# Kernel optimization log

Measured on AMD Instinct MI355X. Metric: run time of the kernel, lower is better.

## Reference

```python
import jax, jax.numpy as jnp
import numpy as np

FEAT = 256
HID = 256
HEADS = 4
DH = HID // HEADS
SCALE = DH ** (-0.5)


def _linear(x, W, b):
    # torch nn.Linear convention: W is [out, in]
    return jnp.einsum('...i,oi->...o', x, W) + b


def _layernorm(x, gamma, beta, eps=1e-5):
    mu = jnp.mean(x, axis=-1, keepdims=True)
    var = jnp.mean(jnp.square(x - mu), axis=-1, keepdims=True)
    return (x - mu) * jax.lax.rsqrt(var + eps) * gamma + beta


def setup_inputs() -> dict:
    key = jax.random.key(0)
    ks = jax.random.split(key, 16)
    B, N = 4, 2048
    def w(k, shape, fan_in):
        return jax.random.uniform(k, shape, jnp.float32, -1.0, 1.0) / np.sqrt(fan_in)
    return {
        'x0': jax.random.normal(ks[0], (B, N, FEAT), jnp.float32),
        'x1': jax.random.normal(ks[1], (B, N, FEAT), jnp.float32),
        'Wqk': w(ks[2], (HID, FEAT), FEAT), 'bqk': w(ks[3], (HID,), FEAT),
        'Wv': w(ks[4], (HID, FEAT), FEAT), 'bv': w(ks[5], (HID,), FEAT),
        'Wp': w(ks[6], (HID, HID), HID), 'bp': w(ks[7], (HID,), HID),
        'W1': w(ks[8], (FEAT * 2, FEAT + HID), FEAT + HID), 'b1': w(ks[9], (FEAT * 2,), FEAT + HID),
        'gamma': jnp.ones((FEAT * 2,), jnp.float32), 'beta': jnp.zeros((FEAT * 2,), jnp.float32),
        'W2': w(ks[10], (FEAT, FEAT * 2), FEAT * 2), 'b2': w(ks[11], (FEAT,), FEAT * 2),
    }


def _forward(x0, x1, Wqk, bqk, Wv, bv, Wp, bp, W1, b1, gamma, beta, W2, b2):
    B, N0, _ = x0.shape
    N1 = x1.shape[1]

    def heads(t):  # [B, N, HID] -> [B, H, N, DH]
        return t.reshape(t.shape[0], t.shape[1], HEADS, DH).transpose(0, 2, 1, 3)

    qk0 = heads(_linear(x0, Wqk, bqk)) * (SCALE ** 0.5)
    qk1 = heads(_linear(x1, Wqk, bqk)) * (SCALE ** 0.5)
    v0 = heads(_linear(x0, Wv, bv))
    v1 = heads(_linear(x1, Wv, bv))

    sim = jnp.einsum('bhid,bhjd->bhij', qk0, qk1)  # [B,H,N0,N1]
    attn01 = jax.nn.softmax(sim, axis=-1)                      # rows over N1
    attn10 = jax.nn.softmax(sim.transpose(0, 1, 3, 2), axis=-1)  # [B,H,N1,N0], rows over N0

    m0 = jnp.einsum('bhij,bhjd->bhid', attn01, v1)  # [B,H,N0,DH]
    m1 = jnp.einsum('bhij,bhjd->bhid', attn10, v0)  # [B,H,N1,DH]

    def merge(t):  # [B,H,N,DH] -> [B,N,HID]
        return t.transpose(0, 2, 1, 3).reshape(t.shape[0], t.shape[2], HID)

    m0 = _linear(merge(m0), Wp, bp)
    m1 = _linear(merge(m1), Wp, bp)

    def mlp(x, m):
        h = _linear(jnp.concatenate([x, m], axis=-1), W1, b1)
        h = jax.nn.gelu(_layernorm(h, gamma, beta), approximate=False)
        return x + _linear(h, W2, b2)

    return mlp(x0, m0), mlp(x1, m1)


def reference(x0, x1, Wqk, bqk, Wv, bv, Wp, bp, W1, b1, gamma, beta, W2, b2):
    return _forward(x0, x1, Wqk, bqk, Wv, bv, Wp, bp, W1, b1, gamma, beta, W2, b2)
```

## Files before the change

kernel.cpp:

```cpp
#include <hip/hip_runtime.h>
#include <hip/hip_bf16.h>
#include <math.h>

typedef __hip_bfloat16 hbf;
typedef __attribute__((ext_vector_type(8))) short short8;
typedef __attribute__((ext_vector_type(4))) short short4v;
typedef __attribute__((ext_vector_type(4))) float f32x4;

#define ROWS 8192
#define SQSL 0.4246609001440095f
#define COFF 24.0f

__device__ __forceinline__ short f2b(float f) {
    union { hbf h; short s; } u; u.h = __float2bfloat16(f); return u.s;
}
__device__ __forceinline__ float b2f(short s) {
    union { unsigned u; float f; } x;
    x.u = ((unsigned)(unsigned short)s) << 16; return x.f;
}

__global__ __launch_bounds__(256)
void prep(const float* __restrict__ Wqk, const float* __restrict__ Wv,
          const float* __restrict__ Wp, const float* __restrict__ W1,
          const float* __restrict__ W2,
          const float* __restrict__ bp, const float* __restrict__ b1,
          short* __restrict__ wq, short* __restrict__ wv,
          short* __restrict__ w1c, short* __restrict__ w2,
          float* __restrict__ bc)
{
    const int bid = blockIdx.x, tid = threadIdx.x;
    if (bid < 512) {
        const float* src; short* dst; int base; float sc = 1.f;
        if (bid < 64)       { src = Wqk; dst = wq; base = bid;       sc = SQSL; }
        else if (bid < 128) { src = Wv;  dst = wv; base = bid - 64; }
        else if (bid < 384) {
            int i = (bid - 128) * 256 + tid;
            int n = i >> 7, c = (i & 127) * 4;
            if (c < 256) {
                float4 f = ((const float4*)W1)[i];
                short4v s;
                s[0] = f2b(f.x); s[1] = f2b(f.y); s[2] = f2b(f.z); s[3] = f2b(f.w);
                *(short4v*)(w1c + (size_t)n * 512 + c) = s;
            }
            return;
        }
        else                { src = W2;  dst = w2; base = bid - 384; }
        int i = base * 256 + tid;
        float4 f = ((const float4*)src)[i];
        short4v s;
        s[0] = f2b(f.x * sc); s[1] = f2b(f.y * sc);
        s[2] = f2b(f.z * sc); s[3] = f2b(f.w * sc);
        *(short4v*)(dst + (size_t)i * 4) = s;
    } else if (bid < 1024) {
        int n = bid - 512;
        const float* wrow = W1 + (size_t)n * 512 + 256;
        float acc = 0.f;
        for (int k = 0; k < 256; ++k)
            acc += wrow[k] * Wp[(size_t)k * 256 + tid];
        w1c[(size_t)n * 512 + 256 + tid] = f2b(acc);
    } else {
        int n = (bid - 1024) * 256 + tid;
        const float* wrow = W1 + (size_t)n * 512 + 256;
        float acc = b1[n];
        for (int k = 0; k < 256; ++k) acc += wrow[k] * bp[k];
        bc[n] = acc;
    }
}

__global__ __launch_bounds__(256)
void gemm_qkv(const float* __restrict__ x0, const float* __restrict__ x1,
              const short* __restrict__ Wa, const short* __restrict__ Wb,
              const float* __restrict__ bias0, const float* __restrict__ bias1,
              short* __restrict__ qkb, short* __restrict__ vtb)
{
    const int fid  = blockIdx.x + (blockIdx.y << 2);
    const int col0 = (fid >> 8) * 128;
    const int row0 = (fid & 255) * 64;
    const int tid = threadIdx.x;
    const int lane = tid & 63, wave = tid >> 6;
    const int ln = lane & 15, quad = lane >> 4;
    const int wm = wave & 1, wn = wave >> 1;

    __shared__ short smem[64 * 72 + 128 * 72];
    short* As = smem;
    short* Bs = smem + 64 * 72;
    short* Vt = smem;

    const int ar = tid >> 2, ac = tid & 3;

    f32x4 acc[2][4];
    #pragma unroll
    for (int i = 0; i < 2; ++i)
        #pragma unroll
        for (int j = 0; j < 4; ++j) acc[i][j] = {0.f, 0.f, 0.f, 0.f};

    const short* wbase = (col0 < 256) ? Wa + (size_t)col0 * 256
                                      : Wb + (size_t)(col0 - 256) * 256;
    const float* xrow = (row0 + ar < ROWS)
        ? x0 + (size_t)(row0 + ar) * 256
        : x1 + (size_t)(row0 + ar - ROWS) * 256;

    float4 aF[4];
    short8 bR[4];
    #pragma unroll
    for (int i = 0; i < 4; ++i) aF[i] = ((const float4*)(xrow + ac * 16))[i];
    bR[0] = *(const short8*)(wbase + (size_t)ar * 256 + ac * 16);
    bR[1] = *(const short8*)(wbase + (size_t)ar * 256 + ac * 16 + 8);
    bR[2] = *(const short8*)(wbase + (size_t)(ar + 64) * 256 + ac * 16);
    bR[3] = *(const short8*)(wbase + (size_t)(ar + 64) * 256 + ac * 16 + 8);

    for (int k0 = 0; k0 < 256; k0 += 64) {
        {
            short8 s0, s1;
            s0[0] = f2b(aF[0].x); s0[1] = f2b(aF[0].y); s0[2] = f2b(aF[0].z); s0[3] = f2b(aF[0].w);
            s0[4] = f2b(aF[1].x); s0[5] = f2b(aF[1].y); s0[6] = f2b(aF[1].z); s0[7] = f2b(aF[1].w);
            s1[0] = f2b(aF[2].x); s1[1] = f2b(aF[2].y); s1[2] = f2b(aF[2].z); s1[3] = f2b(aF[2].w);
            s1[4] = f2b(aF[3].x); s1[5] = f2b(aF[3].y); s1[6] = f2b(aF[3].z); s1[7] = f2b(aF[3].w);
            *(short8*)&As[ar * 72 + ac * 16]     = s0;
            *(short8*)&As[ar * 72 + ac * 16 + 8] = s1;
        }
        *(short8*)&Bs[ar * 72 + ac * 16]            = bR[0];
        *(short8*)&Bs[ar * 72 + ac * 16 + 8]        = bR[1];
        *(short8*)&Bs[(ar + 64) * 72 + ac * 16]     = bR[2];
        *(short8*)&Bs[(ar + 64) * 72 + ac * 16 + 8] = bR[3];
        __syncthreads();

        if (k0 + 64 < 256) {
            const int kk = k0 + 64 + ac * 16;
            #pragma unroll
            for (int i = 0; i < 4; ++i) aF[i] = ((const float4*)(xrow + kk))[i];
            bR[0] = *(const short8*)(wbase + (size_t)ar * 256 + kk);
            bR[1] = *(const short8*)(wbase + (size_t)ar * 256 + kk + 8);
            bR[2] = *(const short8*)(wbase + (size_t)(ar + 64) * 256 + kk);
            bR[3] = *(const short8*)(wbase + (size_t)(ar + 64) * 256 + kk + 8);
        }

        short8 a[2][2], b[4][2];
        #pragma unroll
        for (int mi = 0; mi < 2; ++mi)
            #pragma unroll
            for (int ks = 0; ks < 2; ++ks)
                a[mi][ks] = *(const short8*)&As[(wm * 32 + mi * 16 + ln) * 72 + ks * 32 + quad * 8];
        #pragma unroll
        for (int nj = 0; nj < 4; ++nj)
            #pragma unroll
            for (int ks = 0; ks < 2; ++ks)
                b[nj][ks] = *(const short8*)&Bs[(wn * 64 + nj * 16 + ln) * 72 + ks * 32 + quad * 8];
        #pragma unroll
        for (int mi = 0; mi < 2; ++mi)
            #pragma unroll
            for (int nj = 0; nj < 4; ++nj) {
                acc[mi][nj] = __builtin_amdgcn_mfma_f32_16x16x32_bf16(
                                  b[nj][0], a[mi][0], acc[mi][nj], 0, 0, 0);
                acc[mi][nj] = __builtin_amdgcn_mfma_f32_16x16x32_bf16(
                                  b[nj][1], a[mi][1], acc[mi][nj], 0, 0, 0);
            }
        __syncthreads();
    }

    if (col0 < 256) {
        #pragma unroll
        for (int nj = 0; nj < 4; ++nj) {
            const int wcol = col0 + wn * 64 + nj * 16 + quad * 4;
            float4 bb = *(const float4*)(bias0 + wcol);
            #pragma unroll
            for (int mi = 0; mi < 2; ++mi) {
                const int tok = row0 + wm * 32 + mi * 16 + ln;
                f32x4 v = acc[mi][nj];
                short4v o;
                o[0] = f2b(fmaf(bb.x, SQSL, v[0]));
                o[1] = f2b(fmaf(bb.y, SQSL, v[1]));
                o[2] = f2b(fmaf(bb.z, SQSL, v[2]));
                o[3] = f2b(fmaf(bb.w, SQSL, v[3]));
                *(short4v*)(qkb + (size_t)tok * 256 + wcol) = o;
            }
        }
    } else {
        #pragma unroll
        for (int nj = 0; nj < 4; ++nj) {
            const int wrel = wn * 64 + nj * 16 + quad * 4;
            float4 bb = *(const float4*)(bias1 + (col0 - 256) + wrel);
            #pragma unroll
            for (int mi = 0; mi < 2; ++mi) {
                const int tl = wm * 32 + mi * 16 + ln;
                f32x4 v = acc[mi][nj];
                Vt[(wrel + 0) * 72 + tl] = f2b(v[0] + bb.x);
                Vt[(wrel + 1) * 72 + tl] = f2b(v[1] + bb.y);
                Vt[(wrel + 2) * 72 + tl] = f2b(v[2] + bb.z);
                Vt[(wrel + 3) * 72 + tl] = f2b(v[3] + bb.w);
            }
        }
        __syncthreads();
        {
            const int g4 = (row0 >> 11) * 4, tc0 = row0 & 2047;
            const int r = tid >> 1, hf = tid & 1;
            const int vcol = (col0 - 256) + r;
            const int hh = vcol >> 6, d = vcol & 63;
            short* dst = vtb + (size_t)((g4 + hh) * 64 + d) * 2048 + tc0 + hf * 32;
            #pragma unroll
            for (int cc = 0; cc < 4; ++cc)
                *(short8*)(dst + cc * 8) = *(const short8*)&Vt[r * 72 + hf * 32 + cc * 8];
        }
    }
}

__global__ __launch_bounds__(128, 2)
void attn8(const short* __restrict__ qkb, const short* __restrict__ vtbuf,
           short* __restrict__ pO0, short* __restrict__ pO1,
           float* __restrict__ l0, float* __restrict__ l1)
{
    const int nfl = blockIdx.x + (blockIdx.y << 4) + (blockIdx.z << 8);
    const int qt  = nfl >> 6;
    const int gg  = nfl & 63;
    const int b    = (gg >> 2) & 3, h = gg & 3;
    const int dir  = gg >> 5;
    const int half = (gg >> 4) & 1;
    const int tid = threadIdx.x;
    const int lane = tid & 63, wave = tid >> 6;
    const int ln   = lane & 15, quad = lane >> 4;

    const int qbase = dir * ROWS + b * 2048;
    const int kbase = (1 - dir) * ROWS + b * 2048;
    const int vg    = ((1 - dir) * 4 + b) * 4 + h;
    const int jlo   = half * 1024, jhi = jlo + 1024;

    short* __restrict__ pO = half ? pO1 : pO0;
    float* __restrict__ lb = half ? l1  : l0;

    __shared__ short QP[128 * 72];
    __shared__ short KS[64 * 72];
    __shared__ short VT[64 * 72];

    const int c = tid & 7, r0 = tid >> 3;
    #pragma unroll
    for (int g = 0; g < 8; ++g) {
        int r = r0 + g * 16;
        *(short8*)&QP[r * 72 + c * 8] =
            *(const short8*)(qkb + (size_t)(qbase + qt * 128 + r) * 256 + h * 64 + c * 8);
    }
    #pragma unroll
    for (int g = 0; g < 4; ++g) {
        int r = r0 + g * 16;
        *(short8*)&KS[r * 72 + c * 8] =
            *(const short8*)(qkb + (size_t)(kbase + jlo + r) * 256 + h * 64 + c * 8);
        *(short8*)&VT[r * 72 + c * 8] =
            *(const short8*)(vtbuf + (size_t)(vg * 64 + r) * 2048 + jlo + c * 8);
    }
    __syncthreads();

    short8 qf[4][2];
    #pragma unroll
    for (int mi = 0; mi < 4; ++mi)
        #pragma unroll
        for (int ks = 0; ks < 2; ++ks)
            qf[mi][ks] = *(const short8*)&QP[(wave * 64 + mi * 16 + ln) * 72
                                             + ks * 32 + quad * 8];

    f32x4 Ot[4][4];
    #pragma unroll
    for (int mi = 0; mi < 4; ++mi)
        #pragma unroll
        for (int dt = 0; dt < 4; ++dt) Ot[mi][dt] = {0.f, 0.f, 0.f, 0.f};
    float lrun[4] = {0.f, 0.f, 0.f, 0.f};

    for (int j0 = jlo; j0 < jhi; j0 += 64) {
        short8 kreg[4], vreg[4];
        const bool more = (j0 + 64) < jhi;
        if (more) {
            #pragma unroll
            for (int g = 0; g < 4; ++g) {
                int r = r0 + g * 16;
                kreg[g] = *(const short8*)(qkb + (size_t)(kbase + j0 + 64 + r) * 256
                                           + h * 64 + c * 8);
                vreg[g] = *(const short8*)(vtbuf + (size_t)(vg * 64 + r) * 2048
                                           + j0 + 64 + c * 8);
            }
        }

        f32x4 St[4][4];
        __builtin_amdgcn_s_setprio(1);
        #pragma unroll
        for (int t = 0; t < 4; ++t) {
            short8 k0 = *(const short8*)&KS[(t * 16 + ln) * 72 + quad * 8];
            short8 k1 = *(const short8*)&KS[(t * 16 + ln) * 72 + 32 + quad * 8];
            #pragma unroll
            for (int mi = 0; mi < 4; ++mi) {
                f32x4 z = {0.f, 0.f, 0.f, 0.f};
                z = __builtin_amdgcn_mfma_f32_16x16x32_bf16(k0, qf[mi][0], z, 0, 0, 0);
                St[mi][t] = __builtin_amdgcn_mfma_f32_16x16x32_bf16(k1, qf[mi][1], z, 0, 0, 0);
            }
        }
        __builtin_amdgcn_s_setprio(0);

        float ss[4] = {0.f, 0.f, 0.f, 0.f};
        #pragma unroll
        for (int mi = 0; mi < 4; ++mi)
            #pragma unroll
            for (int t = 0; t < 4; ++t) {
                float p0 = __builtin_amdgcn_exp2f(St[mi][t][0] - COFF);
                float p1 = __builtin_amdgcn_exp2f(St[mi][t][1] - COFF);
                float p2 = __builtin_amdgcn_exp2f(St[mi][t][2] - COFF);
                float p3 = __builtin_amdgcn_exp2f(St[mi][t][3] - COFF);
                ss[mi] += (p0 + p1) + (p2 + p3);
                unsigned d0 = (__float_as_uint(p0) >> 16) |
                              (__float_as_uint(p1) & 0xffff0000u);
                unsigned d1 = (__float_as_uint(p2) >> 16) |
                              (__float_as_uint(p3) & 0xffff0000u);
                *(int2*)&QP[(wave * 64 + mi * 16 + ln) * 72 + t * 16 + quad * 4] =
                    make_int2((int)d0, (int)d1);
            }
        #pragma unroll
        for (int mi = 0; mi < 4; ++mi) {
            float t = ss[mi];
            t += __shfl_xor(t, 16);
            t += __shfl_xor(t, 32);
            lrun[mi] += t;
        }

        short8 pa[4][2];
        #pragma unroll
        for (int mi = 0; mi < 4; ++mi)
            #pragma unroll
            for (int ks = 0; ks < 2; ++ks)
                pa[mi][ks] = *(const short8*)&QP[(wave * 64 + mi * 16 + ln) * 72
                                                 + ks * 32 + quad * 8];
        __builtin_amdgcn_s_setprio(1);
        #pragma unroll
        for (int dt = 0; dt < 4; ++dt) {
            short8 v0 = *(const short8*)&VT[(dt * 16 + ln) * 72 + quad * 8];
            short8 v1 = *(const short8*)&VT[(dt * 16 + ln) * 72 + 32 + quad * 8];
            #pragma unroll
            for (int mi = 0; mi < 4; ++mi) {
                Ot[mi][dt] = __builtin_amdgcn_mfma_f32_16x16x32_bf16(
                                 v0, pa[mi][0], Ot[mi][dt], 0, 0, 0);
                Ot[mi][dt] = __builtin_amdgcn_mfma_f32_16x16x32_bf16(
                                 v1, pa[mi][1], Ot[mi][dt], 0, 0, 0);
            }
        }
        __builtin_amdgcn_s_setprio(0);
        __syncthreads();

        if (more) {
            #pragma unroll
            for (int g = 0; g < 4; ++g) {
                int r = r0 + g * 16;
                *(short8*)&KS[r * 72 + c * 8] = kreg[g];
                *(short8*)&VT[r * 72 + c * 8] = vreg[g];
            }
        }
        __syncthreads();
    }

    #pragma unroll
    for (int mi = 0; mi < 4; ++mi) {
        int tok = qbase + qt * 128 + wave * 64 + mi * 16 + ln;
        if (quad == 0) lb[tok] = lrun[mi];
        #pragma unroll
        for (int dt = 0; dt < 4; ++dt) {
            short4v o;
            #pragma unroll
            for (int r = 0; r < 4; ++r) o[r] = f2b(Ot[mi][dt][r]);
            *(short4v*)(pO + (size_t)tok * 256 + h * 64 + dt * 16 + quad * 4) = o;
        }
    }
}

__global__ __launch_bounds__(256)
void mlp_fused(const float* __restrict__ x0, const float* __restrict__ x1,
               const short* __restrict__ pO0, const short* __restrict__ pO1,
               const float* __restrict__ l0, const float* __restrict__ l1,
               const short* __restrict__ w1c, const short* __restrict__ w2,
               const float* __restrict__ bc, const float* __restrict__ gamma,
               const float* __restrict__ beta, const float* __restrict__ b2,
               float* __restrict__ out)
{
    const int tok0 = blockIdx.x * 32;
    const int tid = threadIdx.x;
    const int lane = tid & 63, wave = tid >> 6;
    const int ln = lane & 15, quad = lane >> 4;

    __shared__ short H [32 * 520];
    __shared__ short Bs[256 * 72];
    __shared__ float stats[4][2][32];

    const int br = tid >> 2, bq = tid & 3;
    short8 bp[8];
    auto loadB = [&](const short* W, int rw, int k0) {
        const short* src = W + (size_t)(rw + br) * 512 + k0 + bq * 16;
        #pragma unroll
        for (int q = 0; q < 4; ++q) {
            bp[2 * q]     = *(const short8*)(src + (size_t)q * 64 * 512);
            bp[2 * q + 1] = *(const short8*)(src + (size_t)q * 64 * 512 + 8);
        }
    };
    loadB(w1c, 0, 0);

    {
        const int arow = tid >> 3, ac = tid & 7;
        const int tok = tok0 + arow;
        if (ac < 4) {
            const float* xr = (tok < ROWS ? x0 + (size_t)tok * 256
                                          : x1 + (size_t)(tok - ROWS) * 256) + ac * 64;
            #pragma unroll
            for (int cc = 0; cc < 8; ++cc) {
                float4 f0 = ((const float4*)(xr + cc * 8))[0];
                float4 f1 = ((const float4*)(xr + cc * 8))[1];
                short8 s;
                s[0] = f2b(f0.x); s[1] = f2b(f0.y); s[2] = f2b(f0.z); s[3] = f2b(f0.w);
                s[4] = f2b(f1.x); s[5] = f2b(f1.y); s[6] = f2b(f1.z); s[7] = f2b(f1.w);
                *(short8*)&H[arow * 520 + ac * 64 + cc * 8] = s;
            }
        } else {
            const int vc = (ac - 4) * 64;
            const float inv = __builtin_amdgcn_rcpf(l0[tok] + l1[tok]);
            #pragma unroll
            for (int cc = 0; cc < 8; ++cc) {
                short8 a = *(const short8*)(pO0 + (size_t)tok * 256 + vc + cc * 8);
                short8 b = *(const short8*)(pO1 + (size_t)tok * 256 + vc + cc * 8);
                short8 s;
                #pragma unroll
                for (int j = 0; j < 8; ++j)
                    s[j] = f2b((b2f(a[j]) + b2f(b[j])) * inv);
                *(short8*)&H[arow * 520 + 256 + vc + cc * 8] = s;
            }
        }
    }

    f32x4 acc[2][8];
    #pragma unroll
    for (int i = 0; i < 2; ++i)
        #pragma unroll
        for (int j = 0; j < 8; ++j) acc[i][j] = {0.f, 0.f, 0.f, 0.f};

    __syncthreads();

    for (int k2 = 0; k2 < 8; ++k2) {
        const int k0 = k2 * 64;
        short8 a0[2], a1[2];
        #pragma unroll
        for (int ks = 0; ks < 2; ++ks) {
            a0[ks] = *(const short8*)&H[ln * 520 + k0 + ks * 32 + quad * 8];
            a1[ks] = *(const short8*)&H[(16 + ln) * 520 + k0 + ks * 32 + quad * 8];
        }
        #pragma unroll
        for (int p = 0; p < 2; ++p) {
            #pragma unroll
            for (int q = 0; q < 4; ++q) {
                *(short8*)&Bs[(br + q * 64) * 72 + bq * 16]     = bp[2 * q];
                *(short8*)&Bs[(br + q * 64) * 72 + bq * 16 + 8] = bp[2 * q + 1];
            }
            __syncthreads();
            if (p == 0)          loadB(w1c, 256, k0);
            else if (k2 < 7)     loadB(w1c, 0, k0 + 64);
            #pragma unroll
            for (int nj = 0; nj < 4; ++nj) {
                #pragma unroll
                for (int ks = 0; ks < 2; ++ks) {
                    short8 bf = *(const short8*)&Bs[(wave * 64 + nj * 16 + ln) * 72
                                                    + ks * 32 + quad * 8];
                    acc[0][p * 4 + nj] = __builtin_amdgcn_mfma_f32_16x16x32_bf16(
                                             bf, a0[ks], acc[0][p * 4 + nj], 0, 0, 0);
                    acc[1][p * 4 + nj] = __builtin_amdgcn_mfma_f32_16x16x32_bf16(
                                             bf, a1[ks], acc[1][p * 4 + nj], 0, 0, 0);
                }
            }
            __syncthreads();
        }
    }

    loadB(w2, 0, 0);

    #pragma unroll
    for (int p = 0; p < 2; ++p)
        #pragma unroll
        for (int nj = 0; nj < 4; ++nj) {
            int hcol = p * 256 + wave * 64 + nj * 16 + quad * 4;
            float4 bb = *(const float4*)(bc + hcol);
            acc[0][p * 4 + nj][0] += bb.x; acc[1][p * 4 + nj][0] += bb.x;
            acc[0][p * 4 + nj][1] += bb.y; acc[1][p * 4 + nj][1] += bb.y;
            acc[0][p * 4 + nj][2] += bb.z; acc[1][p * 4 + nj][2] += bb.z;
            acc[0][p * 4 + nj][3] += bb.w; acc[1][p * 4 + nj][3] += bb.w;
        }

    #pragma unroll
    for (int mi = 0; mi < 2; ++mi) {
        float s1 = 0.f, s2 = 0.f;
        #pragma unroll
        for (int j = 0; j < 8; ++j)
            #pragma unroll
            for (int r = 0; r < 4; ++r) {
                float v = acc[mi][j][r];
                s1 += v; s2 += v * v;
            }
        s1 += __shfl_xor(s1, 16); s2 += __shfl_xor(s2, 16);
        s1 += __shfl_xor(s1, 32); s2 += __shfl_xor(s2, 32);
        if (quad == 0) {
            stats[wave][0][mi * 16 + ln] = s1;
            stats[wave][1][mi * 16 + ln] = s2;
        }
    }
    __syncthreads();

    float mean[2], rstd[2];
    #pragma unroll
    for (int mi = 0; mi < 2; ++mi) {
        int t = mi * 16 + ln;
        float s1 = stats[0][0][t] + stats[1][0][t] + stats[2][0][t] + stats[3][0][t];
        float s2 = stats[0][1][t] + stats[1][1][t] + stats[2][1][t] + stats[3][1][t];
        mean[mi] = s1 * (1.f / 512.f);
        float var = s2 * (1.f / 512.f) - mean[mi] * mean[mi];
        rstd[mi] = rsqrtf(var + 1e-5f);
    }

    #pragma unroll
    for (int p = 0; p < 2; ++p)
        #pragma unroll
        for (int nj = 0; nj < 4; ++nj) {
            int hcol = p * 256 + wave * 64 + nj * 16 + quad * 4;
            float4 gm = *(const float4*)(gamma + hcol);
            float4 bt = *(const float4*)(beta + hcol);
            #pragma unroll
            for (int mi = 0; mi < 2; ++mi) {
                short4v o;
                #pragma unroll
                for (int r = 0; r < 4; ++r) {
                    float g = (r == 0) ? gm.x : (r == 1) ? gm.y : (r == 2) ? gm.z : gm.w;
                    float bta = (r == 0) ? bt.x : (r == 1) ? bt.y : (r == 2) ? bt.z : bt.w;
                    float y = (acc[mi][p * 4 + nj][r] - mean[mi]) * rstd[mi] * g + bta;
                    float u = y * fmaf(y * y, 0.0356774081f, 0.7978845608f);
                    float e = __builtin_amdgcn_exp2f(u * -2.8853900818f);
                    o[r] = f2b(y * __builtin_amdgcn_rcpf(1.f + e));
                }
                *(short4v*)&H[(mi * 16 + ln) * 520 + hcol] = o;
            }
        }

    f32x4 acc2[2][4];
    #pragma unroll
    for (int i = 0; i < 2; ++i)
        #pragma unroll
        for (int j = 0; j < 4; ++j) acc2[i][j] = {0.f, 0.f, 0.f, 0.f};

    for (int s = 0; s < 8; ++s) {
        const int k0 = s * 64;
        #pragma unroll
        for (int q = 0; q < 4; ++q) {
            *(short8*)&Bs[(br + q * 64) * 72 + bq * 16]     = bp[2 * q];
            *(short8*)&Bs[(br + q * 64) * 72 + bq * 16 + 8] = bp[2 * q + 1];
        }
        __syncthreads();
        if (s < 7) loadB(w2, 0, k0 + 64);
        short8 h0[2], h1[2];
        #pragma unroll
        for (int ks = 0; ks < 2; ++ks) {
            h0[ks] = *(const short8*)&H[ln * 520 + k0 + ks * 32 + quad * 8];
            h1[ks] = *(const short8*)&H[(16 + ln) * 520 + k0 + ks * 32 + quad * 8];
        }
        #pragma unroll
        for (int nj = 0; nj < 4; ++nj) {
            #pragma unroll
            for (int ks = 0; ks < 2; ++ks) {
                short8 wf = *(const short8*)&Bs[(wave * 64 + nj * 16 + ln) * 72
                                                + ks * 32 + quad * 8];
                acc2[0][nj] = __builtin_amdgcn_mfma_f32_16x16x32_bf16(
                                  wf, h0[ks], acc2[0][nj], 0, 0, 0);
                acc2[1][nj] = __builtin_amdgcn_mfma_f32_16x16x32_bf16(
                                  wf, h1[ks], acc2[1][nj], 0, 0, 0);
            }
        }
        __syncthreads();
    }

    #pragma unroll
    for (int nj = 0; nj < 4; ++nj) {
        int ocol = wave * 64 + nj * 16 + quad * 4;
        float4 bb = *(const float4*)(b2 + ocol);
        #pragma unroll
        for (int mi = 0; mi < 2; ++mi) {
            int tok = tok0 + mi * 16 + ln;
            const float* xr = (tok < ROWS ? x0 + (size_t)tok * 256
                                          : x1 + (size_t)(tok - ROWS) * 256);
            float4 rv = *(const float4*)(xr + ocol);
            float4 o;
            o.x = acc2[mi][nj][0] + bb.x + rv.x;
            o.y = acc2[mi][nj][1] + bb.y + rv.y;
            o.z = acc2[mi][nj][2] + bb.z + rv.z;
            o.w = acc2[mi][nj][3] + bb.w + rv.w;
            *(float4*)(out + (size_t)tok * 256 + ocol) = o;
        }
    }
}

extern "C" void kernel_launch(void* const* d_in, const int* in_sizes, int n_in,
                              void* d_out, int out_size, void* d_ws, size_t ws_size,
                              hipStream_t stream)
{
    const float* x0    = (const float*)d_in[0];
    const float* x1    = (const float*)d_in[1];
    const float* Wqk   = (const float*)d_in[2];
    const float* bqk   = (const float*)d_in[3];
    const float* Wv    = (const float*)d_in[4];
    const float* bv    = (const float*)d_in[5];
    const float* Wp    = (const float*)d_in[6];
    const float* bp    = (const float*)d_in[7];
    const float* W1    = (const float*)d_in[8];
    const float* b1    = (const float*)d_in[9];
    const float* gamma = (const float*)d_in[10];
    const float* beta  = (const float*)d_in[11];
    const float* W2    = (const float*)d_in[12];
    const float* b2    = (const float*)d_in[13];
    float* out = (float*)d_out;

    char* ws = (char*)d_ws;
    const size_t MB = 1024 * 1024;
    short* qkb  = (short*)ws;
    short* vtb  = (short*)(ws + 8  * MB);
    short* pO0  = (short*)(ws + 16 * MB);
    short* pO1  = (short*)(ws + 24 * MB);
    float* l0   = (float*)(ws + 32 * MB);
    float* l1   = l0 + 16384;
    float* bc   = l1 + 16384;
    short* wq   = (short*)(bc + 512);
    short* wv   = wq + 65536;
    short* w1c  = wv + 65536;
    short* w2   = w1c + 262144;

    prep<<<1026, 256, 0, stream>>>(Wqk, Wv, Wp, W1, W2, bp, b1,
                                   wq, wv, w1c, w2, bc);
    gemm_qkv<<<dim3(4, 256), 256, 0, stream>>>(x0, x1, wq, wv, bqk, bv, qkb, vtb);
    attn8<<<dim3(16, 16, 4), 128, 0, stream>>>(qkb, vtb, pO0, pO1, l0, l1);
    mlp_fused<<<512, 256, 0, stream>>>(x0, x1, pO0, pO1, l0, l1, w1c, w2, bc,
                                       gamma, beta, b2, out);
}
```

Baseline: 202.2 us.

## Load GEMM operands directly into registers and compute softmax row sums with MFMA

The QKV projection and both MLP GEMMs stop staging weights and activations through shared memory. Each wave now loads its MFMA fragments straight from global memory into double-buffered registers, which removes most __syncthreads barriers and LDS traffic. The attention kernel drops the constant exp offset and the setprio hints, computes row sums by an MFMA against a ones vector instead of shuffle reductions, and packs bf16 pairs with a perm instruction. QKV blocks are remapped for locality and launch_bounds now request two blocks per CU. The trade-offs are more redundant global loads, higher register pressure, and a possible exp overflow risk now that the offset is gone.

```diff
diff --git a/kernel.cpp b/kernel.cpp
--- a/kernel.cpp
+++ b/kernel.cpp
@@ -9,7 +9,6 @@
 
 #define ROWS 8192
 #define SQSL 0.4246609001440095f
-#define COFF 24.0f
 
 __device__ __forceinline__ short f2b(float f) {
     union { hbf h; short s; } u; u.h = __float2bfloat16(f); return u.s;
@@ -67,95 +66,98 @@
     }
 }
 
-__global__ __launch_bounds__(256)
+__global__ __launch_bounds__(256, 2)
 void gemm_qkv(const float* __restrict__ x0, const float* __restrict__ x1,
               const short* __restrict__ Wa, const short* __restrict__ Wb,
               const float* __restrict__ bias0, const float* __restrict__ bias1,
               short* __restrict__ qkb, short* __restrict__ vtb)
 {
     const int fid  = blockIdx.x + (blockIdx.y << 2);
-    const int col0 = (fid >> 8) * 128;
-    const int row0 = (fid & 255) * 64;
+    const int col0 = ((fid >> 3) & 3) * 128;
+    const int row0 = ((fid & 7) + (fid >> 5) * 8) * 64;
     const int tid = threadIdx.x;
     const int lane = tid & 63, wave = tid >> 6;
     const int ln = lane & 15, quad = lane >> 4;
     const int wm = wave & 1, wn = wave >> 1;
 
-    __shared__ short smem[64 * 72 + 128 * 72];
-    short* As = smem;
-    short* Bs = smem + 64 * 72;
-    short* Vt = smem;
-
-    const int ar = tid >> 2, ac = tid & 3;
-
-    f32x4 acc[2][4];
-    #pragma unroll
-    for (int i = 0; i < 2; ++i)
-        #pragma unroll
-        for (int j = 0; j < 4; ++j) acc[i][j] = {0.f, 0.f, 0.f, 0.f};
-
+    __shared__ short Vt[128 * 72];
+
+    const float* xr[2];
+    #pragma unroll
+    for (int mi = 0; mi < 2; ++mi) {
+        int r = row0 + wm * 32 + mi * 16 + ln;
+        xr[mi] = ((r < ROWS) ? x0 + (size_t)r * 256
+                             : x1 + (size_t)(r - ROWS) * 256) + quad * 8;
+    }
     const short* wbase = (col0 < 256) ? Wa + (size_t)col0 * 256
                                       : Wb + (size_t)(col0 - 256) * 256;
-    const float* xrow = (row0 + ar < ROWS)
-        ? x0 + (size_t)(row0 + ar) * 256
-        : x1 + (size_t)(row0 + ar - ROWS) * 256;
-
-    float4 aF[4];
-    short8 bR[4];
-    #pragma unroll
-    for (int i = 0; i < 4; ++i) aF[i] = ((const float4*)(xrow + ac * 16))[i];
-    bR[0] = *(const short8*)(wbase + (size_t)ar * 256 + ac * 16);
-    bR[1] = *(const short8*)(wbase + (size_t)ar * 256 + ac * 16 + 8);
-    bR[2] = *(const short8*)(wbase + (size_t)(ar + 64) * 256 + ac * 16);
-    bR[3] = *(const short8*)(wbase + (size_t)(ar + 64) * 256 + ac * 16 + 8);
-
-    for (int k0 = 0; k0 < 256; k0 += 64) {
-        {
-            short8 s0, s1;
-            s0[0] = f2b(aF[0].x); s0[1] = f2b(aF[0].y); s0[2] = f2b(aF[0].z); s0[3] = f2b(aF[0].w);
-            s0[4] = f2b(aF[1].x); s0[5] = f2b(aF[1].y); s0[6] = f2b(aF[1].z); s0[7] = f2b(aF[1].w);
-            s1[0] = f2b(aF[2].x); s1[1] = f2b(aF[2].y); s1[2] = f2b(aF[2].z); s1[3] = f2b(aF[2].w);
-            s1[4] = f2b(aF[3].x); s1[5] = f2b(aF[3].y); s1[6] = f2b(aF[3].z); s1[7] = f2b(aF[3].w);
-            *(short8*)&As[ar * 72 + ac * 16]     = s0;
-            *(short8*)&As[ar * 72 + ac * 16 + 8] = s1;
-        }
-        *(short8*)&Bs[ar * 72 + ac * 16]            = bR[0];
-        *(short8*)&Bs[ar * 72 + ac * 16 + 8]        = bR[1];
-        *(short8*)&Bs[(ar + 64) * 72 + ac * 16]     = bR[2];
-        *(short8*)&Bs[(ar + 64) * 72 + ac * 16 + 8] = bR[3];
-        __syncthreads();
-
-        if (k0 + 64 < 256) {
-            const int kk = k0 + 64 + ac * 16;
-            #pragma unroll
-            for (int i = 0; i < 4; ++i) aF[i] = ((const float4*)(xrow + kk))[i];
-            bR[0] = *(const short8*)(wbase + (size_t)ar * 256 + kk);
-            bR[1] = *(const short8*)(wbase + (size_t)ar * 256 + kk + 8);
-            bR[2] = *(const short8*)(wbase + (size_t)(ar + 64) * 256 + kk);
-            bR[3] = *(const short8*)(wbase + (size_t)(ar + 64) * 256 + kk + 8);
-        }
-
-        short8 a[2][2], b[4][2];
+    const short* wr[4];
+    #pragma unroll
+    for (int nj = 0; nj < 4; ++nj)
+        wr[nj] = wbase + (size_t)(wn * 64 + nj * 16 + ln) * 256 + quad * 8;
+
+    f32x4 acc[2][4];
+    #pragma unroll
+    for (int i = 0; i < 2; ++i)
+        #pragma unroll
+        for (int j = 0; j < 4; ++j) acc[i][j] = {0.f, 0.f, 0.f, 0.f};
+
+    float4 aB[2][2][2][2];
+    short8 bB[2][4][2];
+
+    #pragma unroll
+    for (int mi = 0; mi < 2; ++mi)
+        #pragma unroll
+        for (int ks = 0; ks < 2; ++ks) {
+            const float* p = xr[mi] + ks * 32;
+            aB[0][mi][ks][0] = ((const float4*)p)[0];
+            aB[0][mi][ks][1] = ((const float4*)p)[1];
+        }
+    #pragma unroll
+    for (int nj = 0; nj < 4; ++nj)
+        #pragma unroll
+        for (int ks = 0; ks < 2; ++ks)
+            bB[0][nj][ks] = *(const short8*)(wr[nj] + ks * 32);
+
+    #pragma unroll
+    for (int kk = 0; kk < 4; ++kk) {
+        const int cur = kk & 1, nxt = cur ^ 1;
+        if (kk < 3) {
+            const int k0 = (kk + 1) * 64;
+            #pragma unroll
+            for (int mi = 0; mi < 2; ++mi)
+                #pragma unroll
+                for (int ks = 0; ks < 2; ++ks) {
+                    const float* p = xr[mi] + k0 + ks * 32;
+                    aB[nxt][mi][ks][0] = ((const float4*)p)[0];
+                    aB[nxt][mi][ks][1] = ((const float4*)p)[1];
+                }
+            #pragma unroll
+            for (int nj = 0; nj < 4; ++nj)
+                #pragma unroll
+                for (int ks = 0; ks < 2; ++ks)
+                    bB[nxt][nj][ks] = *(const short8*)(wr[nj] + k0 + ks * 32);
+        }
+        short8 a[2][2];
         #pragma unroll
         for (int mi = 0; mi < 2; ++mi)
             #pragma unroll
-            for (int ks = 0; ks < 2; ++ks)
-                a[mi][ks] = *(const short8*)&As[(wm * 32 + mi * 16 + ln) * 72 + ks * 32 + quad * 8];
-        #pragma unroll
-        for (int nj = 0; nj < 4; ++nj)
-            #pragma unroll
-            for (int ks = 0; ks < 2; ++ks)
-                b[nj][ks] = *(const short8*)&Bs[(wn * 64 + nj * 16 + ln) * 72 + ks * 32 + quad * 8];
+            for (int ks = 0; ks < 2; ++ks) {
+                float4 f0 = aB[cur][mi][ks][0], f1 = aB[cur][mi][ks][1];
+                short8 s;
+                s[0] = f2b(f0.x); s[1] = f2b(f0.y); s[2] = f2b(f0.z); s[3] = f2b(f0.w);
+                s[4] = f2b(f1.x); s[5] = f2b(f1.y); s[6] = f2b(f1.z); s[7] = f2b(f1.w);
+                a[mi][ks] = s;
+            }
         #pragma unroll
         for (int mi = 0; mi < 2; ++mi)
             #pragma unroll
             for (int nj = 0; nj < 4; ++nj) {
                 acc[mi][nj] = __builtin_amdgcn_mfma_f32_16x16x32_bf16(
-                                  b[nj][0], a[mi][0], acc[mi][nj], 0, 0, 0);
+                                  bB[cur][nj][0], a[mi][0], acc[mi][nj], 0, 0, 0);
                 acc[mi][nj] = __builtin_amdgcn_mfma_f32_16x16x32_bf16(
-                                  b[nj][1], a[mi][1], acc[mi][nj], 0, 0, 0);
-            }
-        __syncthreads();
+                                  bB[cur][nj][1], a[mi][1], acc[mi][nj], 0, 0, 0);
+            }
     }
 
     if (col0 < 256) {
@@ -256,12 +258,18 @@
             qf[mi][ks] = *(const short8*)&QP[(wave * 64 + mi * 16 + ln) * 72
                                              + ks * 32 + quad * 8];
 
+    short8 ones;
+    #pragma unroll
+    for (int j = 0; j < 8; ++j) ones[j] = (short)0x3F80;
+
     f32x4 Ot[4][4];
     #pragma unroll
     for (int mi = 0; mi < 4; ++mi)
         #pragma unroll
         for (int dt = 0; dt < 4; ++dt) Ot[mi][dt] = {0.f, 0.f, 0.f, 0.f};
-    float lrun[4] = {0.f, 0.f, 0.f, 0.f};
+    f32x4 lacc[4];
+    #pragma unroll
+    for (int mi = 0; mi < 4; ++mi) lacc[mi] = {0.f, 0.f, 0.f, 0.f};
 
     for (int j0 = jlo; j0 < jhi; j0 += 64) {
         short8 kreg[4], vreg[4];
@@ -278,7 +286,6 @@
         }
 
         f32x4 St[4][4];
-        __builtin_amdgcn_s_setprio(1);
         #pragma unroll
         for (int t = 0; t < 4; ++t) {
             short8 k0 = *(const short8*)&KS[(t * 16 + ln) * 72 + quad * 8];
@@ -290,32 +297,22 @@
                 St[mi][t] = __builtin_amdgcn_mfma_f32_16x16x32_bf16(k1, qf[mi][1], z, 0, 0, 0);
             }
         }
-        __builtin_amdgcn_s_setprio(0);
-
-        float ss[4] = {0.f, 0.f, 0.f, 0.f};
+
         #pragma unroll
         for (int mi = 0; mi < 4; ++mi)
             #pragma unroll
             for (int t = 0; t < 4; ++t) {
-                float p0 = __builtin_amdgcn_exp2f(St[mi][t][0] - COFF);
-                float p1 = __builtin_amdgcn_exp2f(St[mi][t][1] - COFF);
-                float p2 = __builtin_amdgcn_exp2f(St[mi][t][2] - COFF);
-                float p3 = __builtin_amdgcn_exp2f(St[mi][t][3] - COFF);
-                ss[mi] += (p0 + p1) + (p2 + p3);
-                unsigned d0 = (__float_as_uint(p0) >> 16) |
-                              (__float_as_uint(p1) & 0xffff0000u);
-                unsigned d1 = (__float_as_uint(p2) >> 16) |
-                              (__float_as_uint(p3) & 0xffff0000u);
+                float p0 = __builtin_amdgcn_exp2f(St[mi][t][0]);
+                float p1 = __builtin_amdgcn_exp2f(St[mi][t][1]);
+                float p2 = __builtin_amdgcn_exp2f(St[mi][t][2]);
+                float p3 = __builtin_amdgcn_exp2f(St[mi][t][3]);
+                unsigned d0 = __builtin_amdgcn_perm(__float_as_uint(p1),
+                                                    __float_as_uint(p0), 0x07060302u);
+                unsigned d1 = __builtin_amdgcn_perm(__float_as_uint(p3),
+                                                    __float_as_uint(p2), 0x07060302u);
                 *(int2*)&QP[(wave * 64 + mi * 16 + ln) * 72 + t * 16 + quad * 4] =
                     make_int2((int)d0, (int)d1);
             }
-        #pragma unroll
-        for (int mi = 0; mi < 4; ++mi) {
-            float t = ss[mi];
-            t += __shfl_xor(t, 16);
-            t += __shfl_xor(t, 32);
-            lrun[mi] += t;
-        }
 
         short8 pa[4][2];
         #pragma unroll
@@ -324,7 +321,13 @@
             for (int ks = 0; ks < 2; ++ks)
                 pa[mi][ks] = *(const short8*)&QP[(wave * 64 + mi * 16 + ln) * 72
                                                  + ks * 32 + quad * 8];
-        __builtin_amdgcn_s_setprio(1);
+        #pragma unroll
+        for (int mi = 0; mi < 4; ++mi) {
+            lacc[mi] = __builtin_amdgcn_mfma_f32_16x16x32_bf16(
+                           ones, pa[mi][0], lacc[mi], 0, 0, 0);
+            lacc[mi] = __builtin_amdgcn_mfma_f32_16x16x32_bf16(
+                           ones, pa[mi][1], lacc[mi], 0, 0, 0);
+        }
         #pragma unroll
         for (int dt = 0; dt < 4; ++dt) {
             short8 v0 = *(const short8*)&VT[(dt * 16 + ln) * 72 + quad * 8];
@@ -337,7 +340,6 @@
                                  v1, pa[mi][1], Ot[mi][dt], 0, 0, 0);
             }
         }
-        __builtin_amdgcn_s_setprio(0);
         __syncthreads();
 
         if (more) {
@@ -354,7 +356,7 @@
     #pragma unroll
     for (int mi = 0; mi < 4; ++mi) {
         int tok = qbase + qt * 128 + wave * 64 + mi * 16 + ln;
-        if (quad == 0) lb[tok] = lrun[mi];
+        if (quad == 0) lb[tok] = lacc[mi][0];
         #pragma unroll
         for (int dt = 0; dt < 4; ++dt) {
             short4v o;
@@ -365,7 +367,7 @@
     }
 }
 
-__global__ __launch_bounds__(256)
+__global__ __launch_bounds__(256, 2)
 void mlp_fused(const float* __restrict__ x0, const float* __restrict__ x1,
                const short* __restrict__ pO0, const short* __restrict__ pO1,
                const float* __restrict__ l0, const float* __restrict__ l1,
@@ -380,20 +382,18 @@
     const int ln = lane & 15, quad = lane >> 4;
 
     __shared__ short H [32 * 520];
-    __shared__ short Bs[256 * 72];
     __shared__ float stats[4][2][32];
 
-    const int br = tid >> 2, bq = tid & 3;
-    short8 bp[8];
-    auto loadB = [&](const short* W, int rw, int k0) {
-        const short* src = W + (size_t)(rw + br) * 512 + k0 + bq * 16;
-        #pragma unroll
-        for (int q = 0; q < 4; ++q) {
-            bp[2 * q]     = *(const short8*)(src + (size_t)q * 64 * 512);
-            bp[2 * q + 1] = *(const short8*)(src + (size_t)q * 64 * 512 + 8);
-        }
+    short8 bf[2][8];
+    auto loadsec = [&](short8* dst, const short* W, int rowbase, int k0) {
+        #pragma unroll
+        for (int nj = 0; nj < 4; ++nj)
+            #pragma unroll
+            for (int ks = 0; ks < 2; ++ks)
+                dst[nj * 2 + ks] = *(const short8*)(
+                    W + (size_t)(rowbase + nj * 16 + ln) * 512 + k0 + ks * 32 + quad * 8);
     };
-    loadB(w1c, 0, 0);
+    loadsec(bf[0], w1c, wave * 64, 0);
 
     {
         const int arow = tid >> 3, ac = tid & 7;
@@ -434,41 +434,34 @@
 
     __syncthreads();
 
-    for (int k2 = 0; k2 < 8; ++k2) {
-        const int k0 = k2 * 64;
-        short8 a0[2], a1[2];
-        #pragma unroll
-        for (int ks = 0; ks < 2; ++ks) {
-            a0[ks] = *(const short8*)&H[ln * 520 + k0 + ks * 32 + quad * 8];
-            a1[ks] = *(const short8*)&H[(16 + ln) * 520 + k0 + ks * 32 + quad * 8];
-        }
-        #pragma unroll
-        for (int p = 0; p < 2; ++p) {
-            #pragma unroll
-            for (int q = 0; q < 4; ++q) {
-                *(short8*)&Bs[(br + q * 64) * 72 + bq * 16]     = bp[2 * q];
-                *(short8*)&Bs[(br + q * 64) * 72 + bq * 16 + 8] = bp[2 * q + 1];
-            }
-            __syncthreads();
-            if (p == 0)          loadB(w1c, 256, k0);
-            else if (k2 < 7)     loadB(w1c, 0, k0 + 64);
-            #pragma unroll
-            for (int nj = 0; nj < 4; ++nj) {
-                #pragma unroll
-                for (int ks = 0; ks < 2; ++ks) {
-                    short8 bf = *(const short8*)&Bs[(wave * 64 + nj * 16 + ln) * 72
-                                                    + ks * 32 + quad * 8];
-                    acc[0][p * 4 + nj] = __builtin_amdgcn_mfma_f32_16x16x32_bf16(
-                                             bf, a0[ks], acc[0][p * 4 + nj], 0, 0, 0);
-                    acc[1][p * 4 + nj] = __builtin_amdgcn_mfma_f32_16x16x32_bf16(
-                                             bf, a1[ks], acc[1][p * 4 + nj], 0, 0, 0);
-                }
-            }
-            __syncthreads();
-        }
-    }
-
-    loadB(w2, 0, 0);
+    short8 a0[2], a1[2];
+    #pragma unroll
+    for (int s = 0; s < 16; ++s) {
+        const int p = s & 1, k0 = (s >> 1) * 64;
+        if (p == 0) {
+            #pragma unroll
+            for (int ks = 0; ks < 2; ++ks) {
+                a0[ks] = *(const short8*)&H[ln * 520 + k0 + ks * 32 + quad * 8];
+                a1[ks] = *(const short8*)&H[(16 + ln) * 520 + k0 + ks * 32 + quad * 8];
+            }
+        }
+        if (s < 15) {
+            const int sn = s + 1;
+            loadsec(bf[sn & 1], w1c, (sn & 1) * 256 + wave * 64, (sn >> 1) * 64);
+        }
+        #pragma unroll
+        for (int nj = 0; nj < 4; ++nj)
+            #pragma unroll
+            for (int ks = 0; ks < 2; ++ks) {
+                short8 w = bf[s & 1][nj * 2 + ks];
+                acc[0][p * 4 + nj] = __builtin_amdgcn_mfma_f32_16x16x32_bf16(
+                                         w, a0[ks], acc[0][p * 4 + nj], 0, 0, 0);
+                acc[1][p * 4 + nj] = __builtin_amdgcn_mfma_f32_16x16x32_bf16(
+                                         w, a1[ks], acc[1][p * 4 + nj], 0, 0, 0);
+            }
+    }
+
+    loadsec(bf[0], w2, wave * 64, 0);
 
     #pragma unroll
     for (int p = 0; p < 2; ++p)
@@ -534,6 +527,7 @@
                 *(short4v*)&H[(mi * 16 + ln) * 520 + hcol] = o;
             }
         }
+    __syncthreads();
 
     f32x4 acc2[2][4];
     #pragma unroll
@@ -541,34 +535,26 @@
         #pragma unroll
         for (int j = 0; j < 4; ++j) acc2[i][j] = {0.f, 0.f, 0.f, 0.f};
 
+    #pragma unroll
     for (int s = 0; s < 8; ++s) {
         const int k0 = s * 64;
-        #pragma unroll
-        for (int q = 0; q < 4; ++q) {
-            *(short8*)&Bs[(br + q * 64) * 72 + bq * 16]     = bp[2 * q];
-            *(short8*)&Bs[(br + q * 64) * 72 + bq * 16 + 8] = bp[2 * q + 1];
-        }
-        __syncthreads();
-        if (s < 7) loadB(w2, 0, k0 + 64);
         short8 h0[2], h1[2];
         #pragma unroll
         for (int ks = 0; ks < 2; ++ks) {
             h0[ks] = *(const short8*)&H[ln * 520 + k0 + ks * 32 + quad * 8];
             h1[ks] = *(const short8*)&H[(16 + ln) * 520 + k0 + ks * 32 + quad * 8];
         }
-        #pragma unroll
-        for (int nj = 0; nj < 4; ++nj) {
+        if (s < 7) loadsec(bf[(s + 1) & 1], w2, wave * 64, k0 + 64);
+        #pragma unroll
+        for (int nj = 0; nj < 4; ++nj)
             #pragma unroll
             for (int ks = 0; ks < 2; ++ks) {
-                short8 wf = *(const short8*)&Bs[(wave * 64 + nj * 16 + ln) * 72
-                                                + ks * 32 + quad * 8];
+                short8 w = bf[s & 1][nj * 2 + ks];
                 acc2[0][nj] = __builtin_amdgcn_mfma_f32_16x16x32_bf16(
-                                  wf, h0[ks], acc2[0][nj], 0, 0, 0);
+                                  w, h0[ks], acc2[0][nj], 0, 0, 0);
                 acc2[1][nj] = __builtin_amdgcn_mfma_f32_16x16x32_bf16(
-                                  wf, h1[ks], acc2[1][nj], 0, 0, 0);
-            }
-        }
-        __syncthreads();
+                                  w, h1[ks], acc2[1][nj], 0, 0, 0);
+            }
     }
 
     #pragma unroll
```

Measured after the change: 235.9 us. 16.6% more time.
